# Performance work log

Hardware: AMD Instinct MI355X
Metric: run time of the kernel (lower is better)

## Reference

```python
import jax, jax.numpy as jnp
import numpy as np

IMG_SIZE = 500
FM = 31
RATIOS = [1.0, 2.0, 0.5]
SCALES = [128, 256, 512]
PRE_NMS_TOPN = 1000
POST_NMS_TOPN = 256
IOU_THR = 0.8
VARIANCES = np.array([0.1, 0.1, 0.2, 0.2], np.float32)
BATCH = 64
TOTAL_ANCHORS = FM * FM * len(RATIOS) * len(SCALES)  # 8649


def _generate_anchors():
    # mimics bbox_utils.generate_anchors: normalized grid centers + base sizes
    stride = 1.0 / FM
    ctr = (np.arange(FM, dtype=np.float32) / FM) + stride / 2.0
    gy, gx = np.meshgrid(ctr, ctr, indexing="ij")
    base = []
    for scale in SCALES:
        for ratio in RATIOS:
            w = scale * np.sqrt(ratio) / IMG_SIZE
            h = scale / np.sqrt(ratio) / IMG_SIZE
            base.append([-h / 2, -w / 2, h / 2, w / 2])
    base = np.array(base, np.float32)                        # [9, 4]
    ctrs = np.stack([gy, gx, gy, gx], -1).reshape(-1, 1, 4)  # [FM*FM, 1, 4]
    anc = (ctrs + base[None]).reshape(-1, 4)                 # [8649, 4] yxyx
    return np.clip(anc, 0.0, 1.0)


def setup_inputs() -> dict:
    key = jax.random.key(0)
    k1, k2, k3 = jax.random.split(key, 3)
    return {
        "rpn_bbox_deltas": jax.random.normal(k1, (BATCH, TOTAL_ANCHORS, 4), jnp.float32),
        "rpn_probs": jax.random.uniform(k2, (BATCH, TOTAL_ANCHORS), dtype=jnp.float32),
        "gt_labels": jax.random.randint(k3, (BATCH, 10), 0, 21, jnp.int32),
        "anchors": jnp.asarray(_generate_anchors()),
    }


def _delta_to_bbox(anchors, deltas):
    # anchors [A,4] yxyx broadcast against deltas [B,A,4] (ty,tx,th,tw)
    ah = anchors[..., 2] - anchors[..., 0]
    aw = anchors[..., 3] - anchors[..., 1]
    acy = anchors[..., 0] + 0.5 * ah
    acx = anchors[..., 1] + 0.5 * aw
    h = jnp.exp(deltas[..., 2]) * ah
    w = jnp.exp(deltas[..., 3]) * aw
    cy = deltas[..., 0] * ah + acy
    cx = deltas[..., 1] * aw + acx
    return jnp.stack([cy - 0.5 * h, cx - 0.5 * w, cy + 0.5 * h, cx + 0.5 * w], axis=-1)


def _pairwise_iou(b):
    # b [N,4] yxyx -> [N,N]
    area = (b[:, 2] - b[:, 0]) * (b[:, 3] - b[:, 1])
    y1 = jnp.maximum(b[:, None, 0], b[None, :, 0])
    x1 = jnp.maximum(b[:, None, 1], b[None, :, 1])
    y2 = jnp.minimum(b[:, None, 2], b[None, :, 2])
    x2 = jnp.minimum(b[:, None, 3], b[None, :, 3])
    inter = jnp.maximum(y2 - y1, 0.0) * jnp.maximum(x2 - x1, 0.0)
    union = area[:, None] + area[None, :] - inter
    return inter / jnp.maximum(union, 1e-8)


def _nms_single(boxes, scores):
    # boxes [N,4] already sorted by descending score (from top_k);
    # greedy NMS matching single-class tf.image.combined_non_max_suppression
    n = boxes.shape[0]
    iou = _pairwise_iou(boxes)
    idx = jnp.arange(n)

    def body(keep, i):
        sup = keep[i] & (iou[i] > IOU_THR) & (idx > i)
        return keep & ~sup, None

    keep, _ = jax.lax.scan(body, jnp.ones((n,), bool), jnp.arange(n))
    masked = jnp.where(keep, scores, -1.0)  # scores are probs >= 0
    sel_scores, sel_idx = jax.lax.top_k(masked, POST_NMS_TOPN)
    sel_boxes = jnp.clip(boxes[sel_idx], 0.0, 1.0)  # combined NMS clips boxes
    valid = sel_scores >= 0.0
    return (jnp.where(valid[:, None], sel_boxes, 0.0),
            jnp.where(valid, sel_scores, 0.0))


def reference(rpn_bbox_deltas, rpn_probs, gt_labels, anchors):
    deltas = rpn_bbox_deltas * jnp.asarray(VARIANCES)          # [B,A,4]
    rpn_bboxes = _delta_to_bbox(anchors[None], deltas)         # [B,A,4]
    pre_scores, pre_idx = jax.lax.top_k(rpn_probs, PRE_NMS_TOPN)  # [B,1000]
    pre_boxes = jnp.take_along_axis(rpn_bboxes, pre_idx[..., None], axis=1)
    roi_bboxes, roi_scores = jax.vmap(_nms_single)(pre_boxes, pre_scores)
    return roi_bboxes, roi_scores  # [B,256,4], [B,256]
```

## Files before the change

### kernel.cpp

```cpp
#include <hip/hip_runtime.h>
#include <math.h>

#define BATCH 64
#define A_TOTAL 8649
#define PRE 1000
#define POST 256
#define NBINS 4096
#define NW 16
#define TRIG 120
#define TRIP 65
#define TRI_WORDS (TRIG * TRIP)

__global__ __launch_bounds__(1024) void k_topk_decode(
    const float* __restrict__ deltas,
    const float* __restrict__ probs,
    const float* __restrict__ anchors,
    float4* __restrict__ tboxes,
    float* __restrict__ tscores,
    float* __restrict__ tareas)
{
    #pragma clang fp contract(off)
    const int b = blockIdx.x;
    const int t = threadIdx.x;
    __shared__ unsigned int hist[NBINS];
    __shared__ unsigned int exc[NBINS];
    __shared__ unsigned int sbits[A_TOTAL];
    __shared__ unsigned long long cand[2048];
    __shared__ unsigned int gsum[256];
    __shared__ unsigned int s_thr;
    __shared__ unsigned int s_n;

    for (int i = t; i < NBINS; i += 1024) hist[i] = 0u;
    __syncthreads();

    const float* pr = probs + (size_t)b * A_TOTAL;
    for (int i = t; i < A_TOTAL; i += 1024) {
        unsigned int bits = __float_as_uint(pr[i]);
        sbits[i] = bits;
        atomicAdd(&hist[bits >> 18], 1u);
    }
    __syncthreads();

    if (t < 256) {
        unsigned int gs = 0;
        #pragma unroll
        for (int q = 0; q < 16; ++q) gs += hist[t * 16 + q];
        gsum[t] = gs;
    }
    __syncthreads();
    if (t < 64) {
        const int l = t;
        unsigned int a  = gsum[4 * l];
        unsigned int b2 = gsum[4 * l + 1];
        unsigned int c  = gsum[4 * l + 2];
        unsigned int d  = gsum[4 * l + 3];
        unsigned int quad = a + b2 + c + d;
        unsigned int q = quad;
        #pragma unroll
        for (int off = 1; off < 64; off <<= 1) {
            unsigned int v = __shfl_down(q, off);
            q += (l + off < 64) ? v : 0u;
        }
        gsum[4 * l]     = q;
        gsum[4 * l + 1] = q - a;
        gsum[4 * l + 2] = q - a - b2;
        gsum[4 * l + 3] = q - a - b2 - c;
    }
    __syncthreads();
    if (t < 256) {
        unsigned int run = (t == 255) ? 0u : gsum[t + 1];
        for (int q = 15; q >= 0; --q) {
            int bin = t * 16 + q;
            exc[bin] = run;
            run += hist[bin];
        }
    }
    __syncthreads();
    for (int bin = t; bin < NBINS; bin += 1024) {
        unsigned int ge = exc[bin] + hist[bin];
        unsigned int ge1 = (bin == NBINS - 1) ? 0u : (exc[bin + 1] + hist[bin + 1]);
        if (ge >= PRE && ge1 < PRE) { s_thr = (unsigned int)bin; s_n = ge; }
    }
    __syncthreads();
    const unsigned int T = s_thr;
    const int n = (s_n > 2048u) ? 2048 : (int)s_n;
    for (int i = t; i < NBINS; i += 1024) hist[i] = 0u;
    __syncthreads();

    for (int i = t; i < A_TOTAL; i += 1024) {
        unsigned int bits = sbits[i];
        unsigned int bin = bits >> 18;
        if (bin >= T) {
            unsigned int p = exc[bin] + atomicAdd(&hist[bin], 1u);
            if (p < 2048u)
                cand[p] = ((unsigned long long)bits << 32) |
                          (unsigned long long)(0xFFFFFFFFu - (unsigned int)i);
        }
    }
    __syncthreads();

    const float4* anc4 = (const float4*)anchors;
    const float4* dl4  = (const float4*)(deltas + (size_t)b * A_TOTAL * 4);
    for (int p = t; p < n; p += 1024) {
        unsigned long long key = cand[p];
        unsigned int bin = (unsigned int)(key >> 50);
        int segs = (int)exc[bin];
        int sege = (bin > 0) ? (int)exc[bin - 1] : n;
        if (sege > 2048) sege = 2048;
        unsigned int rank = (unsigned int)segs;
        for (int q = segs; q < sege; ++q) rank += (cand[q] > key);
        if (rank >= PRE) continue;
        unsigned int idx = 0xFFFFFFFFu - (unsigned int)(key & 0xFFFFFFFFull);
        float sc = __uint_as_float((unsigned int)(key >> 32));
        float4 a = anc4[idx];
        float4 d = dl4[idx];
        float ah  = a.z - a.x;
        float aw  = a.w - a.y;
        float acy = a.x + 0.5f * ah;
        float acx = a.y + 0.5f * aw;
        float ty = d.x * 0.1f, tx = d.y * 0.1f, th = d.z * 0.2f, tw = d.w * 0.2f;
        float h = (float)exp((double)th) * ah;
        float w = (float)exp((double)tw) * aw;
        float cy = ty * ah + acy;
        float cx = tx * aw + acx;
        float4 bx = make_float4(cy - 0.5f * h, cx - 0.5f * w, cy + 0.5f * h, cx + 0.5f * w);
        tboxes[(size_t)b * PRE + rank] = bx;
        tscores[(size_t)b * PRE + rank] = sc;
        tareas[(size_t)b * PRE + rank] = (bx.z - bx.x) * (bx.w - bx.y);
    }
}

__global__ __launch_bounds__(256) void k_masks(
    const float4* __restrict__ tboxes,
    const float* __restrict__ tareas,
    unsigned long long* __restrict__ mtri,
    unsigned long long* __restrict__ mdiag)
{
    #pragma clang fp contract(off)
    const int b = blockIdx.y;
    int f = blockIdx.x * 4 + (threadIdx.x >> 6);
    f = __builtin_amdgcn_readfirstlane(f);
    int I = 0;
    while (f >= 16 - I) { f -= 16 - I; ++I; }
    const int W = I + f;
    const int lane = threadIdx.x & 63;
    const int row = (I << 6) + lane;
    const int rr = (row < PRE) ? row : 0;
    const float4 bi = tboxes[(size_t)b * PRE + rr];
    const float areai = tareas[(size_t)b * PRE + rr];
    const float4* __restrict__ bjp = tboxes + (size_t)b * PRE + (W << 6);
    const float*  __restrict__ ajp = tareas + (size_t)b * PRE + (W << 6);
    const int jmax = (PRE - (W << 6) < 64) ? (PRE - (W << 6)) : 64;
    const double C = (double)0.8f + 0x1p-25;
    const bool diag = (I == W);
    unsigned int mlo = 0u, mhi = 0u;

#define IOU_SUP(jj, sup) do { \
        const float4 bj = bjp[jj]; \
        const float aj = ajp[jj]; \
        float y1 = fmaxf(bi.x, bj.x); \
        float x1 = fmaxf(bi.y, bj.y); \
        float y2 = fminf(bi.z, bj.z); \
        float x2 = fminf(bi.w, bj.w); \
        float inter = fmaxf(y2 - y1, 0.0f) * fmaxf(x2 - x1, 0.0f); \
        float uni = (areai + aj) - inter;             \
        float u = fmaxf(uni, 1e-8f); \
        sup = ((double)inter >= C * (double)u);       \
        if (diag) sup = sup && (lane < (jj)); \
    } while (0)

    if (jmax == 64) {
        #pragma unroll 4
        for (int jj = 0; jj < 32; ++jj) {
            bool sup; IOU_SUP(jj, sup);
            mlo |= sup ? (1u << jj) : 0u;
        }
        #pragma unroll 4
        for (int jj = 32; jj < 64; ++jj) {
            bool sup; IOU_SUP(jj, sup);
            mhi |= sup ? (1u << (jj - 32)) : 0u;
        }
    } else {
        for (int jj = 0; jj < jmax; ++jj) {
            bool sup; IOU_SUP(jj, sup);
            unsigned int s = sup ? (1u << (jj & 31)) : 0u;
            if (jj < 32) mlo |= s; else mhi |= s;
        }
    }
#undef IOU_SUP
    const unsigned long long mword =
        ((unsigned long long)mhi << 32) | (unsigned long long)mlo;
    if (row < PRE) {
        if (diag) {
            mdiag[((size_t)b << 10) + (W << 6) + lane] = mword;
        } else {
            const int cg = 15 * I - (I * (I - 1)) / 2 + (W - I - 1);
            mtri[(size_t)b * TRI_WORDS + (size_t)cg * TRIP + lane] = mword;
        }
    }
}

__global__ __launch_bounds__(512) void k_nms_out(
    const float4* __restrict__ tboxes,
    const float* __restrict__ tscores,
    const unsigned long long* __restrict__ mtri,
    const unsigned long long* __restrict__ mdiag,
    float* __restrict__ out)
{
    #pragma clang fp contract(off)
    const int b = blockIdx.x;
    const int tid = threadIdx.x;
    __shared__ __align__(16) unsigned long long Ml[TRI_WORDS];
    __shared__ int sidx[POST];
    __shared__ int s_kc;

    unsigned int dlo[NW], dhi[NW];
    if (tid < 64) {
        const int lane = tid;
        const unsigned long long* Db = mdiag + ((size_t)b << 10);
        #pragma unroll
        for (int W = 0; W < NW; ++W) {
            const int base = W << 6;
            const int nvalid = (PRE - base < 64) ? (PRE - base) : 64;
            unsigned long long dv = Db[base + lane];
            if (lane >= nvalid) dv = 0ull;
            dlo[W] = (unsigned int)dv;
            dhi[W] = (unsigned int)(dv >> 32);
        }
    }

    {
        const float4* src = (const float4*)(mtri + (size_t)b * TRI_WORDS);
        float4* dst = (float4*)Ml;
        for (int idx = tid; idx < TRI_WORDS / 2; idx += 512) dst[idx] = src[idx];
    }
    __syncthreads();

    if (tid < 64) {
        const int lane = tid;
        const int wword = lane & 15;
        const int wgrp  = lane >> 4;
        unsigned long long rm = 0ull;
        int kc = 0;
        bool done = false;
        #pragma unroll
        for (int W = 0; W < NW; ++W) {
            const int base = W << 6;
            unsigned int rlo = (unsigned int)__builtin_amdgcn_readlane((int)(unsigned int)rm, W)
                             | (unsigned int)__builtin_amdgcn_readlane((int)(unsigned int)rm, W + 16)
                             | (unsigned int)__builtin_amdgcn_readlane((int)(unsigned int)rm, W + 32)
                             | (unsigned int)__builtin_amdgcn_readlane((int)(unsigned int)rm, W + 48);
            unsigned int rhi = (unsigned int)__builtin_amdgcn_readlane((int)(unsigned int)(rm >> 32), W)
                             | (unsigned int)__builtin_amdgcn_readlane((int)(unsigned int)(rm >> 32), W + 16)
                             | (unsigned int)__builtin_amdgcn_readlane((int)(unsigned int)(rm >> 32), W + 32)
                             | (unsigned int)__builtin_amdgcn_readlane((int)(unsigned int)(rm >> 32), W + 48);
            unsigned long long rmW = ((unsigned long long)rhi << 32) | (unsigned long long)rlo;
            unsigned long long valid = (PRE - base >= 64) ? ~0ull : ((1ull << (PRE - base)) - 1ull);
            unsigned long long alive = ~rmW & valid;
            unsigned long long keptw = 0ull;
            while (alive) {
                int i = __builtin_amdgcn_readfirstlane(__ffsll(alive) - 1);
                keptw |= (1ull << i);
                if (lane == 0) sidx[kc] = base + i;
                ++kc;
                if (kc == POST) { done = true; break; }
                unsigned int dl = (unsigned int)__builtin_amdgcn_readlane((int)dlo[W], i);
                unsigned int dh = (unsigned int)__builtin_amdgcn_readlane((int)dhi[W], i);
                unsigned long long d = ((unsigned long long)dh << 32) | (unsigned long long)dl;
                alive &= ~(d | (1ull << i));
            }
            if (done) break;
            const int cgW = 15 * W - (W * (W - 1)) / 2;
            unsigned long long kw = keptw;
            while (kw) {
                unsigned long long tA = kw;
                if (wgrp > 0) tA &= tA - 1ull;
                if (wgrp > 1) tA &= tA - 1ull;
                if (wgrp > 2) tA &= tA - 1ull;
                const bool vA = (tA != 0ull);
                const int iA = vA ? (__ffsll(tA) - 1) : 0;
                unsigned long long kw2 = kw;
                kw2 &= kw2 - 1ull; kw2 &= kw2 - 1ull; kw2 &= kw2 - 1ull; kw2 &= kw2 - 1ull;
                unsigned long long tB = kw2;
                if (wgrp > 0) tB &= tB - 1ull;
                if (wgrp > 1) tB &= tB - 1ull;
                if (wgrp > 2) tB &= tB - 1ull;
                const bool vB = (tB != 0ull);
                const int iB = vB ? (__ffsll(tB) - 1) : 0;
                kw = kw2;
                kw &= kw - 1ull; kw &= kw - 1ull; kw &= kw - 1ull; kw &= kw - 1ull;
                unsigned long long lA = 0ull, lB = 0ull;
                if (wword > W) {
                    const int col = cgW + (wword - W - 1);
                    lA = Ml[col * TRIP + iA];
                    lB = Ml[col * TRIP + iB];
                }
                unsigned long long gA =
                    ((unsigned long long)(unsigned int)__builtin_amdgcn_readlane((int)dhi[W], iA) << 32)
                  |  (unsigned long long)(unsigned int)__builtin_amdgcn_readlane((int)dlo[W], iA);
                unsigned long long gB =
                    ((unsigned long long)(unsigned int)__builtin_amdgcn_readlane((int)dhi[W], iB) << 32)
                  |  (unsigned long long)(unsigned int)__builtin_amdgcn_readlane((int)dlo[W], iB);
                unsigned long long mA = (wword > W) ? lA : ((wword == W) ? gA : 0ull);
                unsigned long long mB = (wword > W) ? lB : ((wword == W) ? gB : 0ull);
                if (!vA) mA = 0ull;
                if (!vB) mB = 0ull;
                rm |= mA | mB;
            }
        }
        if (tid == 0) s_kc = kc;
    }
    __syncthreads();

    const int kc = s_kc;
    const float4* bb = tboxes + (size_t)b * PRE;
    const float* ss = tscores + (size_t)b * PRE;
    float4* oB = (float4*)out + (size_t)b * POST;
    float* oS = out + (size_t)BATCH * POST * 4 + (size_t)b * POST;
    for (int t2 = tid; t2 < POST; t2 += 512) {
        float4 v = make_float4(0.f, 0.f, 0.f, 0.f);
        float sc = 0.f;
        if (t2 < kc) {
            int r = sidx[t2];
            float4 bx = bb[r];
            v.x = fminf(fmaxf(bx.x, 0.f), 1.f);
            v.y = fminf(fmaxf(bx.y, 0.f), 1.f);
            v.z = fminf(fmaxf(bx.z, 0.f), 1.f);
            v.w = fminf(fmaxf(bx.w, 0.f), 1.f);
            sc = ss[r];
        }
        oB[t2] = v;
        oS[t2] = sc;
    }
}

extern "C" void kernel_launch(void* const* d_in, const int* in_sizes, int n_in,
                              void* d_out, int out_size, void* d_ws, size_t ws_size,
                              hipStream_t stream) {
    const float* deltas  = (const float*)d_in[0];
    const float* probs   = (const float*)d_in[1];
    const float* anchors = (const float*)d_in[3];
    float* out = (float*)d_out;

    char* ws = (char*)d_ws;
    float4* tboxes = (float4*)ws;
    float* tscores = (float*)(ws + 1024000);
    float* tareas  = (float*)(ws + 1280000);
    unsigned long long* mdiag = (unsigned long long*)(ws + 1536000);
    unsigned long long* mtri  = (unsigned long long*)(ws + 2060288);

    k_topk_decode<<<dim3(BATCH), dim3(1024), 0, stream>>>(deltas, probs, anchors,
                                                          tboxes, tscores, tareas);
    k_masks<<<dim3(34, BATCH), dim3(256), 0, stream>>>(tboxes, tareas, mtri, mdiag);
    k_nms_out<<<dim3(BATCH), dim3(512), 0, stream>>>(tboxes, tscores, mtri, mdiag, out);
}
```

Before: 89.30 us.

## Broadcast column boxes via readlane, drop areas buffer, simplify NMS mask propagation

The mask kernel now loads each column tile's boxes once per lane and broadcasts them with readlane instead of reloading them per iteration. Box areas are recomputed on the fly, so the separate areas buffer and its global writes and reads are gone. In the NMS kernel the diagonal masks are staged into shared memory, and the propagation loop walks the newly kept indices from sidx four at a time, replacing the bit-peeling readlane logic. The aim is fewer global loads and simpler serial NMS code, at the cost of extra shared memory and readlane-heavy inner loops.

```diff
diff --git a/kernel.cpp b/kernel.cpp
--- a/kernel.cpp
+++ b/kernel.cpp
@@ -16,8 +16,7 @@
     const float* __restrict__ probs,
     const float* __restrict__ anchors,
     float4* __restrict__ tboxes,
-    float* __restrict__ tscores,
-    float* __restrict__ tareas)
+    float* __restrict__ tscores)
 {
     #pragma clang fp contract(off)
     const int b = blockIdx.x;
@@ -126,13 +125,11 @@
         float4 bx = make_float4(cy - 0.5f * h, cx - 0.5f * w, cy + 0.5f * h, cx + 0.5f * w);
         tboxes[(size_t)b * PRE + rank] = bx;
         tscores[(size_t)b * PRE + rank] = sc;
-        tareas[(size_t)b * PRE + rank] = (bx.z - bx.x) * (bx.w - bx.y);
     }
 }
 
 __global__ __launch_bounds__(256) void k_masks(
     const float4* __restrict__ tboxes,
-    const float* __restrict__ tareas,
     unsigned long long* __restrict__ mtri,
     unsigned long long* __restrict__ mdiag)
 {
@@ -145,49 +142,39 @@
     const int W = I + f;
     const int lane = threadIdx.x & 63;
     const int row = (I << 6) + lane;
-    const int rr = (row < PRE) ? row : 0;
+    const int rr = (row < PRE) ? row : (PRE - 1);
     const float4 bi = tboxes[(size_t)b * PRE + rr];
-    const float areai = tareas[(size_t)b * PRE + rr];
-    const float4* __restrict__ bjp = tboxes + (size_t)b * PRE + (W << 6);
-    const float*  __restrict__ ajp = tareas + (size_t)b * PRE + (W << 6);
-    const int jmax = (PRE - (W << 6) < 64) ? (PRE - (W << 6)) : 64;
+    const float areai = (bi.z - bi.x) * (bi.w - bi.y);
+    const int Jbase = W << 6;
+    const int jr = Jbase + lane;
+    const int jrr = (jr < PRE) ? jr : (PRE - 1);
+    const float4 bjv = tboxes[(size_t)b * PRE + jrr];
+    const float areajv = (bjv.z - bjv.x) * (bjv.w - bjv.y);
+    const int jmax = (PRE - Jbase < 64) ? (PRE - Jbase) : 64;
     const double C = (double)0.8f + 0x1p-25;
     const bool diag = (I == W);
     unsigned int mlo = 0u, mhi = 0u;
 
-#define IOU_SUP(jj, sup) do { \
-        const float4 bj = bjp[jj]; \
-        const float aj = ajp[jj]; \
-        float y1 = fmaxf(bi.x, bj.x); \
-        float x1 = fmaxf(bi.y, bj.y); \
-        float y2 = fminf(bi.z, bj.z); \
-        float x2 = fminf(bi.w, bj.w); \
-        float inter = fmaxf(y2 - y1, 0.0f) * fmaxf(x2 - x1, 0.0f); \
-        float uni = (areai + aj) - inter;             \
-        float u = fmaxf(uni, 1e-8f); \
-        sup = ((double)inter >= C * (double)u);       \
-        if (diag) sup = sup && (lane < (jj)); \
-    } while (0)
-
-    if (jmax == 64) {
-        #pragma unroll 4
-        for (int jj = 0; jj < 32; ++jj) {
-            bool sup; IOU_SUP(jj, sup);
-            mlo |= sup ? (1u << jj) : 0u;
-        }
-        #pragma unroll 4
-        for (int jj = 32; jj < 64; ++jj) {
-            bool sup; IOU_SUP(jj, sup);
-            mhi |= sup ? (1u << (jj - 32)) : 0u;
-        }
-    } else {
-        for (int jj = 0; jj < jmax; ++jj) {
-            bool sup; IOU_SUP(jj, sup);
-            unsigned int s = sup ? (1u << (jj & 31)) : 0u;
-            if (jj < 32) mlo |= s; else mhi |= s;
-        }
-    }
-#undef IOU_SUP
+    #pragma unroll 4
+    for (int jj = 0; jj < jmax; ++jj) {
+        float sx = __int_as_float(__builtin_amdgcn_readlane(__float_as_int(bjv.x), jj));
+        float sy = __int_as_float(__builtin_amdgcn_readlane(__float_as_int(bjv.y), jj));
+        float sz = __int_as_float(__builtin_amdgcn_readlane(__float_as_int(bjv.z), jj));
+        float sw = __int_as_float(__builtin_amdgcn_readlane(__float_as_int(bjv.w), jj));
+        float sa = __int_as_float(__builtin_amdgcn_readlane(__float_as_int(areajv), jj));
+        float y1 = fmaxf(bi.x, sx);
+        float x1 = fmaxf(bi.y, sy);
+        float y2 = fminf(bi.z, sz);
+        float x2 = fminf(bi.w, sw);
+        float inter = fmaxf(y2 - y1, 0.0f) * fmaxf(x2 - x1, 0.0f);
+        float uni = (areai + sa) - inter;
+        float u = fmaxf(uni, 1e-8f);
+        bool sup = ((double)inter >= C * (double)u);
+        if (diag) sup = sup && (lane < jj);
+        unsigned int s = sup ? 1u : 0u;
+        if (jj < 32) mlo |= (s << jj); else mhi |= (s << (jj - 32));
+    }
+
     const unsigned long long mword =
         ((unsigned long long)mhi << 32) | (unsigned long long)mlo;
     if (row < PRE) {
@@ -211,19 +198,19 @@
     const int b = blockIdx.x;
     const int tid = threadIdx.x;
     __shared__ __align__(16) unsigned long long Ml[TRI_WORDS];
+    __shared__ __align__(16) unsigned long long Mdl[NW * 64];
     __shared__ int sidx[POST];
     __shared__ int s_kc;
 
     unsigned int dlo[NW], dhi[NW];
     if (tid < 64) {
-        const int lane = tid;
         const unsigned long long* Db = mdiag + ((size_t)b << 10);
         #pragma unroll
         for (int W = 0; W < NW; ++W) {
             const int base = W << 6;
             const int nvalid = (PRE - base < 64) ? (PRE - base) : 64;
-            unsigned long long dv = Db[base + lane];
-            if (lane >= nvalid) dv = 0ull;
+            unsigned long long dv = Db[base + tid];
+            if (tid >= nvalid) dv = 0ull;
             dlo[W] = (unsigned int)dv;
             dhi[W] = (unsigned int)(dv >> 32);
         }
@@ -232,7 +219,10 @@
     {
         const float4* src = (const float4*)(mtri + (size_t)b * TRI_WORDS);
         float4* dst = (float4*)Ml;
-        for (int idx = tid; idx < TRI_WORDS / 2; idx += 512) dst[idx] = src[idx];
+        for (int i = tid; i < TRI_WORDS / 2; i += 512) dst[i] = src[i];
+        const float4* src2 = (const float4*)(mdiag + ((size_t)b << 10));
+        float4* dst2 = (float4*)Mdl;
+        for (int i = tid; i < (NW * 64) / 2; i += 512) dst2[i] = src2[i];
     }
     __syncthreads();
 
@@ -257,10 +247,9 @@
             unsigned long long rmW = ((unsigned long long)rhi << 32) | (unsigned long long)rlo;
             unsigned long long valid = (PRE - base >= 64) ? ~0ull : ((1ull << (PRE - base)) - 1ull);
             unsigned long long alive = ~rmW & valid;
-            unsigned long long keptw = 0ull;
+            const int k0 = kc;
             while (alive) {
                 int i = __builtin_amdgcn_readfirstlane(__ffsll(alive) - 1);
-                keptw |= (1ull << i);
                 if (lane == 0) sidx[kc] = base + i;
                 ++kc;
                 if (kc == POST) { done = true; break; }
@@ -271,44 +260,18 @@
             }
             if (done) break;
             const int cgW = 15 * W - (W * (W - 1)) / 2;
-            unsigned long long kw = keptw;
-            while (kw) {
-                unsigned long long tA = kw;
-                if (wgrp > 0) tA &= tA - 1ull;
-                if (wgrp > 1) tA &= tA - 1ull;
-                if (wgrp > 2) tA &= tA - 1ull;
-                const bool vA = (tA != 0ull);
-                const int iA = vA ? (__ffsll(tA) - 1) : 0;
-                unsigned long long kw2 = kw;
-                kw2 &= kw2 - 1ull; kw2 &= kw2 - 1ull; kw2 &= kw2 - 1ull; kw2 &= kw2 - 1ull;
-                unsigned long long tB = kw2;
-                if (wgrp > 0) tB &= tB - 1ull;
-                if (wgrp > 1) tB &= tB - 1ull;
-                if (wgrp > 2) tB &= tB - 1ull;
-                const bool vB = (tB != 0ull);
-                const int iB = vB ? (__ffsll(tB) - 1) : 0;
-                kw = kw2;
-                kw &= kw - 1ull; kw &= kw - 1ull; kw &= kw - 1ull; kw &= kw - 1ull;
-                unsigned long long lA = 0ull, lB = 0ull;
-                if (wword > W) {
-                    const int col = cgW + (wword - W - 1);
-                    lA = Ml[col * TRIP + iA];
-                    lB = Ml[col * TRIP + iB];
+            for (int fp = k0; fp < kc; fp += 4) {
+                const int idx = fp + wgrp;
+                unsigned long long m = 0ull;
+                if (idx < kc) {
+                    const int ii = sidx[idx] & 63;
+                    if (wword > W)       m = Ml[(cgW + wword - W - 1) * TRIP + ii];
+                    else if (wword == W) m = Mdl[(W << 6) + ii];
                 }
-                unsigned long long gA =
-                    ((unsigned long long)(unsigned int)__builtin_amdgcn_readlane((int)dhi[W], iA) << 32)
-                  |  (unsigned long long)(unsigned int)__builtin_amdgcn_readlane((int)dlo[W], iA);
-                unsigned long long gB =
-                    ((unsigned long long)(unsigned int)__builtin_amdgcn_readlane((int)dhi[W], iB) << 32)
-                  |  (unsigned long long)(unsigned int)__builtin_amdgcn_readlane((int)dlo[W], iB);
-                unsigned long long mA = (wword > W) ? lA : ((wword == W) ? gA : 0ull);
-                unsigned long long mB = (wword > W) ? lB : ((wword == W) ? gB : 0ull);
-                if (!vA) mA = 0ull;
-                if (!vB) mB = 0ull;
-                rm |= mA | mB;
+                rm |= m;
             }
         }
-        if (tid == 0) s_kc = kc;
+        if (lane == 0) s_kc = kc;
     }
     __syncthreads();
 
@@ -345,12 +308,11 @@
     char* ws = (char*)d_ws;
     float4* tboxes = (float4*)ws;
     float* tscores = (float*)(ws + 1024000);
-    float* tareas  = (float*)(ws + 1280000);
-    unsigned long long* mdiag = (unsigned long long*)(ws + 1536000);
-    unsigned long long* mtri  = (unsigned long long*)(ws + 2060288);
+    unsigned long long* mdiag = (unsigned long long*)(ws + 1280000);
+    unsigned long long* mtri  = (unsigned long long*)(ws + 1804288);
 
     k_topk_decode<<<dim3(BATCH), dim3(1024), 0, stream>>>(deltas, probs, anchors,
-                                                          tboxes, tscores, tareas);
-    k_masks<<<dim3(34, BATCH), dim3(256), 0, stream>>>(tboxes, tareas, mtri, mdiag);
+                                                          tboxes, tscores);
+    k_masks<<<dim3(34, BATCH), dim3(256), 0, stream>>>(tboxes, mtri, mdiag);
     k_nms_out<<<dim3(BATCH), dim3(512), 0, stream>>>(tboxes, tscores, mtri, mdiag, out);
 }
```

After: 94.48 us. 5.8% more time.
